# Kernel tuning notes

Measured on AMD Instinct MI355X. Metric: run time of the kernel, lower is better.

Reference implementation:

```python
import jax, jax.numpy as jnp
import numpy as np

N_NODES = 100000
N_EDGES = 1600000
N_FEAT = 128
N_HID = 128


def cheb_conv_k2(x, edge_index, W0, W1, b):
    """PyG ChebConv with K=2, sym norm, lambda_max=2.0.
    Reduces to: out = x @ W0 + (L_hat x) @ W1 + b, where
    L_hat = 2L/lambda_max - I = -D^{-1/2} A D^{-1/2} (diagonal cancels).
    """
    n = x.shape[0]
    row, col = edge_index[0], edge_index[1]
    deg = jax.ops.segment_sum(jnp.ones_like(row, dtype=x.dtype), row, num_segments=n)
    dinv = jnp.where(deg > 0, jax.lax.rsqrt(jnp.maximum(deg, 1.0)), 0.0)
    w = -(dinv[row] * dinv[col])                     # [E] edge weights of L_hat
    tx1 = jax.ops.segment_sum(x[col] * w[:, None], row, num_segments=n)  # [N, F]
    return x @ W0 + tx1 @ W1 + b


def setup_inputs() -> dict:
    key = jax.random.key(0)
    ks = jax.random.split(key, 8)
    glorot = lambda k, fi, fo: jax.random.normal(k, (fi, fo), dtype=jnp.float32) * np.float32(np.sqrt(2.0 / (fi + fo)))
    x = jax.random.normal(ks[0], (N_NODES, N_FEAT), dtype=jnp.float32)
    edge_index = jax.random.randint(ks[1], (2, N_EDGES), 0, N_NODES, dtype=jnp.int64 if jax.config.jax_enable_x64 else jnp.int32)
    return {
        "x": x,
        "edge_index": edge_index,
        "W0_1": glorot(ks[2], N_FEAT, N_HID),
        "W1_1": glorot(ks[3], N_FEAT, N_HID),
        "b1": jnp.zeros((N_HID,), dtype=jnp.float32),
        "W0_2": glorot(ks[4], N_HID, N_HID),
        "W1_2": glorot(ks[5], N_HID, N_HID),
        "b2": jnp.zeros((N_HID,), dtype=jnp.float32),
    }


def reference(x, edge_index, W0_1, W1_1, b1, W0_2, W1_2, b2):
    # eval mode: input Dropout, dropout_adj(p=0.8), and per-layer Dropout are identity
    x1 = jax.nn.relu(cheb_conv_k2(x, edge_index, W0_1, W1_1, b1))
    x2 = jax.nn.relu(cheb_conv_k2(x1, edge_index, W0_2, W1_2, b2))
    # mean of the two layer outputs; outAct is identity
    return (x1 + x2) * 0.5
```

## Files before the change

### kernel.cpp

```cpp
#include <hip/hip_runtime.h>

#define NN 100000
#define NE 1600000
#define NF 128
#define NSTRIP2 (NN / 32)
#define NBUCK ((NN + 127) / 128)
#define CAP 2560
#define CHUNK 8192

typedef __attribute__((ext_vector_type(8))) short short8;
typedef __attribute__((ext_vector_type(4))) float f32x4;

__device__ __forceinline__ unsigned short f2b(float f) {
    union { float f; unsigned int u; } v; v.f = f;
    unsigned int u = v.u;
    unsigned int r = (u + 0x7fffu + ((u >> 16) & 1u)) >> 16;
    return (unsigned short)r;
}
__device__ __forceinline__ unsigned int cvtpk(float lo, float hi) {
    unsigned int r;
    asm("v_cvt_pk_bf16_f32 %0, %1, %2" : "=v"(r) : "v"(lo), "v"(hi));
    return r;
}

__global__ __launch_bounds__(512) void k_bin(const int* __restrict__ row,
                                             const int* __restrict__ col,
                                             int* __restrict__ gcur,
                                             unsigned int* __restrict__ gslab) {
    __shared__ int hist[NBUCK];
    __shared__ int start[NBUCK];
    __shared__ int gbase[NBUCK];
    __shared__ int scanbuf[512];
    __shared__ unsigned int stage[CHUNK];
    __shared__ unsigned short sb[CHUNK];

    const int t = threadIdx.x;
    const int e0 = blockIdx.x * CHUNK;
    const int cnt = min(CHUNK, NE - e0);

    for (int i = t; i < NBUCK; i += 512) hist[i] = 0;
    __syncthreads();
    for (int i = t; i < cnt; i += 512) atomicAdd(&hist[row[e0 + i] >> 7], 1);
    __syncthreads();

    const int b0 = t * 2;
    int s = 0;
#pragma unroll
    for (int k = 0; k < 2; ++k) { int idx = b0 + k; if (idx < NBUCK) s += hist[idx]; }
    scanbuf[t] = s;
    __syncthreads();
    for (int off = 1; off < 512; off <<= 1) {
        int u = t >= off ? scanbuf[t - off] : 0;
        __syncthreads();
        scanbuf[t] += u;
        __syncthreads();
    }
    int run = t > 0 ? scanbuf[t - 1] : 0;
#pragma unroll
    for (int k = 0; k < 2; ++k) {
        int idx = b0 + k;
        if (idx < NBUCK) { start[idx] = run; run += hist[idx]; }
    }
    __syncthreads();

    for (int i = t; i < NBUCK; i += 512) {
        int c = hist[i];
        gbase[i] = c > 0 ? atomicAdd(&gcur[i], c) : 0;
        hist[i] = start[i];
    }
    __syncthreads();

    for (int i = t; i < cnt; i += 512) {
        int r = row[e0 + i];
        int b = r >> 7;
        int p = atomicAdd(&hist[b], 1);
        stage[p] = (unsigned int)col[e0 + i] | ((unsigned int)(r & 127) << 17);
        sb[p] = (unsigned short)b;
    }
    __syncthreads();

    for (int i = t; i < cnt; i += 512) {
        int b = sb[i];
        gslab[gbase[b] + (i - start[b])] = stage[i];
    }
}

__global__ __launch_bounds__(256) void k_csr(const unsigned int* __restrict__ gslab,
                                             const int* __restrict__ gcur,
                                             int* __restrict__ offs,
                                             int* __restrict__ ccol,
                                             float* __restrict__ dinv) {
    __shared__ int rh[128];
    __shared__ int rcur[128];
    __shared__ unsigned int scol[CAP];
    __shared__ int redbuf[256];

    const int b = blockIdx.x;
    const int segbase = b * CAP;
    const int cnt = gcur[b] - segbase;
    const int t = threadIdx.x;

    int partial = 0;
    for (int i = t; i < b; i += 256) partial += gcur[i] - i * CAP;
    redbuf[t] = partial;
    if (t < 128) rh[t] = 0;
    __syncthreads();
    for (int off = 128; off > 0; off >>= 1) {
        if (t < off) redbuf[t] += redbuf[t + off];
        __syncthreads();
    }
    const int csr0 = redbuf[0];

    for (int i = t; i < cnt; i += 256) atomicAdd(&rh[gslab[segbase + i] >> 17], 1);
    __syncthreads();
    if (t == 0) {
        int run = 0;
        for (int r = 0; r < 128; ++r) { rcur[r] = run; run += rh[r]; }
    }
    __syncthreads();

    const int rbase = b * 128;
    if (t < 128 && rbase + t < NN) {
        offs[rbase + t] = csr0 + rcur[t];
        int d = rh[t];
        dinv[rbase + t] = d > 0 ? rsqrtf((float)d) : 0.0f;
    }
    if (b == NBUCK - 1 && t == 0) offs[NN] = NE;
    __syncthreads();

    for (int i = t; i < cnt; i += 256) {
        unsigned int v = gslab[segbase + i];
        int p = atomicAdd(&rcur[v >> 17], 1);
        scol[p] = v & 0x1ffff;
    }
    __syncthreads();
    for (int i = t; i < cnt; i += 256) ccol[csr0 + i] = scol[i];
}

__global__ __launch_bounds__(256) void k_quant(const float* __restrict__ x,
                                               const float* __restrict__ dinv,
                                               unsigned short* __restrict__ xq,
                                               float* __restrict__ dsc,
                                               float* __restrict__ sx) {
    int r = (blockIdx.x * 256 + threadIdx.x) >> 6;
    int lane = threadIdx.x & 63;
    float2 v = ((const float2*)x)[r * 64 + lane];
    float m = fmaxf(fabsf(v.x), fabsf(v.y));
#pragma unroll
    for (int mask = 32; mask; mask >>= 1) m = fmaxf(m, __shfl_xor(m, mask));
    float s = m * (1.0f / 127.0f);
    float inv = m > 0.0f ? 127.0f / m : 0.0f;
    int qx = (int)rintf(v.x * inv) + 128;
    int qy = (int)rintf(v.y * inv) + 128;
    xq[r * 64 + lane] = (unsigned short)(qx | (qy << 8));
    if (lane == 0) { dsc[r] = dinv[r] * s; sx[r] = s; }
}

__global__ __launch_bounds__(256) void k_pack(const float* __restrict__ W01,
                                              const float* __restrict__ W11,
                                              const float* __restrict__ W02,
                                              const float* __restrict__ W12,
                                              unsigned short* __restrict__ WP,
                                              int* __restrict__ gcur) {
    int idx = blockIdx.x * 256 + threadIdx.x;
    if (idx < NBUCK) gcur[idx] = idx * CAP;
    int mi = idx >> 14;
    int e = idx & 16383;
    const float* W = mi == 0 ? W01 : mi == 1 ? W02 : mi == 2 ? W11 : W12;
    int midx = mi == 0 ? 0 : mi == 1 ? 2 : mi == 2 ? 1 : 3;
    int k = e >> 7, n = e & 127;
    int kt = k >> 5, g = (k >> 3) & 3, j = k & 7;
    WP[midx * 16384 + (((kt * 4 + g) * 128 + n) << 3) + j] = f2b(W[e]);
}

__global__ __launch_bounds__(256) void k_gather(const int* __restrict__ offs,
                                                const int* __restrict__ ccol,
                                                const float* __restrict__ dsc,
                                                const float* __restrict__ dinv,
                                                const uint2* __restrict__ xq64,
                                                uint4* __restrict__ txb4,
                                                float qbias) {
    int r = (blockIdx.x * 256 + threadIdx.x) >> 6;
    if (r >= NN) return;
    int lane = threadIdx.x & 63;
    int fl = lane & 15, q = lane >> 4;
    int beg = offs[r], end = offs[r + 1];
    float a0 = 0.f, a1 = 0.f, a2 = 0.f, a3 = 0.f;
    float a4 = 0.f, a5 = 0.f, a6 = 0.f, a7 = 0.f, S = 0.f;
    int j = beg + q;
    for (; j + 12 < end; j += 16) {
        int c0 = ccol[j], c1 = ccol[j + 4], c2 = ccol[j + 8], c3 = ccol[j + 12];
        float w0 = dsc[c0], w1 = dsc[c1], w2 = dsc[c2], w3 = dsc[c3];
        uint2 u0 = xq64[c0 * 16 + fl];
        uint2 u1 = xq64[c1 * 16 + fl];
        uint2 u2 = xq64[c2 * 16 + fl];
        uint2 u3 = xq64[c3 * 16 + fl];
        a0 += w0 * (float)(u0.x & 0xffu)         + w1 * (float)(u1.x & 0xffu)
            + w2 * (float)(u2.x & 0xffu)         + w3 * (float)(u3.x & 0xffu);
        a1 += w0 * (float)((u0.x >> 8) & 0xffu)  + w1 * (float)((u1.x >> 8) & 0xffu)
            + w2 * (float)((u2.x >> 8) & 0xffu)  + w3 * (float)((u3.x >> 8) & 0xffu);
        a2 += w0 * (float)((u0.x >> 16) & 0xffu) + w1 * (float)((u1.x >> 16) & 0xffu)
            + w2 * (float)((u2.x >> 16) & 0xffu) + w3 * (float)((u3.x >> 16) & 0xffu);
        a3 += w0 * (float)(u0.x >> 24)           + w1 * (float)(u1.x >> 24)
            + w2 * (float)(u2.x >> 24)           + w3 * (float)(u3.x >> 24);
        a4 += w0 * (float)(u0.y & 0xffu)         + w1 * (float)(u1.y & 0xffu)
            + w2 * (float)(u2.y & 0xffu)         + w3 * (float)(u3.y & 0xffu);
        a5 += w0 * (float)((u0.y >> 8) & 0xffu)  + w1 * (float)((u1.y >> 8) & 0xffu)
            + w2 * (float)((u2.y >> 8) & 0xffu)  + w3 * (float)((u3.y >> 8) & 0xffu);
        a6 += w0 * (float)((u0.y >> 16) & 0xffu) + w1 * (float)((u1.y >> 16) & 0xffu)
            + w2 * (float)((u2.y >> 16) & 0xffu) + w3 * (float)((u3.y >> 16) & 0xffu);
        a7 += w0 * (float)(u0.y >> 24)           + w1 * (float)(u1.y >> 24)
            + w2 * (float)(u2.y >> 24)           + w3 * (float)(u3.y >> 24);
        S += w0 + w1 + w2 + w3;
    }
    for (; j < end; j += 4) {
        int c = ccol[j];
        float w = dsc[c];
        uint2 u = xq64[c * 16 + fl];
        a0 += w * (float)(u.x & 0xffu);
        a1 += w * (float)((u.x >> 8) & 0xffu);
        a2 += w * (float)((u.x >> 16) & 0xffu);
        a3 += w * (float)(u.x >> 24);
        a4 += w * (float)(u.y & 0xffu);
        a5 += w * (float)((u.y >> 8) & 0xffu);
        a6 += w * (float)((u.y >> 16) & 0xffu);
        a7 += w * (float)(u.y >> 24);
        S += w;
    }
#pragma unroll
    for (int mask = 32; mask >= 16; mask >>= 1) {
        a0 += __shfl_xor(a0, mask); a1 += __shfl_xor(a1, mask);
        a2 += __shfl_xor(a2, mask); a3 += __shfl_xor(a3, mask);
        a4 += __shfl_xor(a4, mask); a5 += __shfl_xor(a5, mask);
        a6 += __shfl_xor(a6, mask); a7 += __shfl_xor(a7, mask);
        S  += __shfl_xor(S, mask);
    }
    if (q == 0) {
        float s = -dinv[r];
        float qb = qbias * S;
        a0 = s * (a0 - qb); a1 = s * (a1 - qb); a2 = s * (a2 - qb); a3 = s * (a3 - qb);
        a4 = s * (a4 - qb); a5 = s * (a5 - qb); a6 = s * (a6 - qb); a7 = s * (a7 - qb);
        uint4 o;
        o.x = cvtpk(a0, a1);
        o.y = cvtpk(a2, a3);
        o.z = cvtpk(a4, a5);
        o.w = cvtpk(a6, a7);
        txb4[r * 16 + fl] = o;
    }
}

__global__ __launch_bounds__(256) void k_mm(const unsigned char* __restrict__ Aq,
                                            const float* __restrict__ s_in,
                                            float qoff,
                                            const unsigned short* __restrict__ Tbf,
                                            const unsigned short* __restrict__ WP0,
                                            const unsigned short* __restrict__ WP1,
                                            const float* __restrict__ bias,
                                            const float* __restrict__ dinv,
                                            float* __restrict__ out,
                                            unsigned char* __restrict__ Qout,
                                            float* __restrict__ dsc_out,
                                            float* __restrict__ s1_out,
                                            int mode) {
    int wid = (blockIdx.x * 256 + threadIdx.x) >> 6;
    if (wid >= NSTRIP2) return;
    int lane = threadIdx.x & 63;
    int g = lane >> 4, m = lane & 15;

    short8 a[2][4], t[2][4];
#pragma unroll
    for (int s = 0; s < 2; ++s) {
        int row = wid * 32 + s * 16 + m;
        float sA = s_in[row];
        float nb = -qoff * sA;
        const unsigned char* Arow = Aq + (size_t)row * NF + g * 8;
        const short8* Tfr = (const short8*)(Tbf + (size_t)row * NF + g * 8);
#pragma unroll
        for (int kt = 0; kt < 4; ++kt) {
            uint2 u = *(const uint2*)(Arow + kt * 32);
            float f0 = fmaf((float)(u.x & 0xffu), sA, nb);
            float f1 = fmaf((float)((u.x >> 8) & 0xffu), sA, nb);
            float f2 = fmaf((float)((u.x >> 16) & 0xffu), sA, nb);
            float f3 = fmaf((float)(u.x >> 24), sA, nb);
            float f4 = fmaf((float)(u.y & 0xffu), sA, nb);
            float f5 = fmaf((float)((u.y >> 8) & 0xffu), sA, nb);
            float f6 = fmaf((float)((u.y >> 16) & 0xffu), sA, nb);
            float f7 = fmaf((float)(u.y >> 24), sA, nb);
            union { uint4 q; short8 v; } cc;
            cc.q.x = cvtpk(f0, f1);
            cc.q.y = cvtpk(f2, f3);
            cc.q.z = cvtpk(f4, f5);
            cc.q.w = cvtpk(f6, f7);
            a[s][kt] = cc.v;
            t[s][kt] = Tfr[kt * 4];
        }
    }

    const short8* B0 = (const short8*)WP0 + g * 128 + m;
    const short8* B1 = (const short8*)WP1 + g * 128 + m;

    f32x4 acc[2][8];
#pragma unroll
    for (int nt = 0; nt < 8; ++nt) {
        float b = bias[nt * 16 + m];
#pragma unroll
        for (int s = 0; s < 2; ++s) {
            acc[s][nt][0] = b; acc[s][nt][1] = b; acc[s][nt][2] = b; acc[s][nt][3] = b;
        }
    }

#pragma unroll
    for (int nt = 0; nt < 8; ++nt) {
#pragma unroll
        for (int kt = 0; kt < 4; ++kt) {
            short8 b0 = B0[kt * 512 + nt * 16];
            short8 b1 = B1[kt * 512 + nt * 16];
#pragma unroll
            for (int s = 0; s < 2; ++s) {
                acc[s][nt] = __builtin_amdgcn_mfma_f32_16x16x32_bf16(a[s][kt], b0, acc[s][nt], 0, 0, 0);
                acc[s][nt] = __builtin_amdgcn_mfma_f32_16x16x32_bf16(t[s][kt], b1, acc[s][nt], 0, 0, 0);
            }
        }
    }

#pragma unroll
    for (int s = 0; s < 2; ++s)
#pragma unroll
        for (int nt = 0; nt < 8; ++nt)
#pragma unroll
            for (int r = 0; r < 4; ++r) acc[s][nt][r] = fmaxf(acc[s][nt][r], 0.0f);

    if (mode == 0) {
#pragma unroll
        for (int s = 0; s < 2; ++s) {
            int rbase = wid * 32 + s * 16 + g * 4;
            float mr[4] = {0.0f, 0.0f, 0.0f, 0.0f};
#pragma unroll
            for (int nt = 0; nt < 8; ++nt)
#pragma unroll
                for (int r = 0; r < 4; ++r) mr[r] = fmaxf(mr[r], acc[s][nt][r]);
#pragma unroll
            for (int mask = 1; mask < 16; mask <<= 1)
#pragma unroll
                for (int r = 0; r < 4; ++r) mr[r] = fmaxf(mr[r], __shfl_xor(mr[r], mask));

            float inv[4], s1v[4];
#pragma unroll
            for (int r = 0; r < 4; ++r) {
                s1v[r] = mr[r] * (1.0f / 255.0f);
                inv[r] = mr[r] > 0.0f ? 255.0f / mr[r] : 0.0f;
            }
#pragma unroll
            for (int nt = 0; nt < 8; ++nt) {
                int c = nt * 16 + m;
#pragma unroll
                for (int r = 0; r < 4; ++r) {
                    int qv = (int)rintf(acc[s][nt][r] * inv[r]);
                    qv = qv > 255 ? 255 : qv;
                    Qout[(size_t)(rbase + r) * NF + c] = (unsigned char)qv;
                }
            }
            if (m == 0) {
#pragma unroll
                for (int r = 0; r < 4; ++r) {
                    s1_out[rbase + r] = s1v[r];
                    dsc_out[rbase + r] = dinv[rbase + r] * s1v[r];
                }
            }
        }
    } else {
#pragma unroll
        for (int s = 0; s < 2; ++s) {
            int rbase = wid * 32 + s * 16 + g * 4;
            float sR[4];
#pragma unroll
            for (int r = 0; r < 4; ++r) sR[r] = s_in[rbase + r];
#pragma unroll
            for (int nt = 0; nt < 8; ++nt) {
                int c = nt * 16 + m;
#pragma unroll
                for (int r = 0; r < 4; ++r) {
                    size_t o = (size_t)(rbase + r) * NF + c;
                    float x1v = sR[r] * (float)Aq[o];
                    out[o] = 0.5f * (x1v + acc[s][nt][r]);
                }
            }
        }
    }
}

extern "C" void kernel_launch(void* const* d_in, const int* in_sizes, int n_in,
                              void* d_out, int out_size, void* d_ws, size_t ws_size,
                              hipStream_t stream) {
    const float* x   = (const float*)d_in[0];
    const int*   ei  = (const int*)d_in[1];
    const float* W01 = (const float*)d_in[2];
    const float* W11 = (const float*)d_in[3];
    const float* b1  = (const float*)d_in[4];
    const float* W02 = (const float*)d_in[5];
    const float* W12 = (const float*)d_in[6];
    const float* b2  = (const float*)d_in[7];
    float* out = (float*)d_out;

    const int* row = ei;
    const int* col = ei + NE;

    char* ws = (char*)d_ws;
    int*            gcur  = (int*)(ws);
    float*          dinv  = (float*)(ws + 6400);
    int*            offs  = (int*)(ws + 406400);
    int*            ccol  = (int*)(ws + 806416);
    unsigned short* WP    = (unsigned short*)(ws + 7206416);
    float*          dsc   = (float*)(ws + 7337488);
    float*          s1a   = (float*)(ws + 7737488);
    float*          sx    = (float*)(ws + 8137488);
    unsigned short* xq    = (unsigned short*)(ws + 8537488);
    unsigned int*   txb   = (unsigned int*)(ws + 21337488);
    unsigned int*   gslab = (unsigned int*)(ws + 21337488);

    unsigned char*  xq8 = (unsigned char*)xq;
    unsigned short* WP01 = WP;
    unsigned short* WP11 = WP + 16384;
    unsigned short* WP02 = WP + 32768;
    unsigned short* WP12 = WP + 49152;

    k_pack <<<(4 * 16384) / 256, 256, 0, stream>>>(W01, W11, W02, W12, WP, gcur);
    k_bin  <<<(NE + CHUNK - 1) / CHUNK, 512, 0, stream>>>(row, col, gcur, gslab);
    k_csr  <<<NBUCK, 256, 0, stream>>>(gslab, gcur, offs, ccol, dinv);

    k_quant<<<(NN * 64) / 256, 256, 0, stream>>>(x, dinv, xq, dsc, sx);

    const int gatherBlocks = (NN * 64) / 256;
    const int mmBlocks = (NSTRIP2 * 64 + 255) / 256;

    k_gather<<<gatherBlocks, 256, 0, stream>>>(offs, ccol, dsc, dinv,
                                               (const uint2*)xq, (uint4*)txb, 128.0f);
    k_mm    <<<mmBlocks, 256, 0, stream>>>(xq8, sx, 128.0f, (const unsigned short*)txb,
                                           WP01, WP11, b1, dinv, out, xq8, dsc, s1a, 0);

    k_gather<<<gatherBlocks, 256, 0, stream>>>(offs, ccol, dsc, dinv,
                                               (const uint2*)xq, (uint4*)txb, 0.0f);
    k_mm    <<<mmBlocks, 256, 0, stream>>>(xq8, s1a, 0.0f, (const unsigned short*)txb,
                                           WP02, WP12, b2, dinv, out, xq8, dsc, s1a, 1);
}
```

Baseline: 226.9 us.

## Stage packed weights in LDS for matmul and batch gather tail loads

The matmul kernel now copies both packed bf16 weight matrices (64 KB) into shared memory once per block and reads MFMA B fragments from LDS instead of global memory. The gather kernel's scalar remainder loop is replaced by one unrolled step that issues up to three independent neighbour loads together. Out-of-range slots point at a sentinel row NN whose dsc entry is set to zero, so workspace offsets shift to make room for it. The LDS staging adds a per-block copy and a large shared allocation that can reduce occupancy. The tail rewrite assumes at most three leftover edges per lane.

Result: faster. 207.2 us (-8.7%).

```diff
diff --git a/kernel.cpp b/kernel.cpp
--- a/kernel.cpp
+++ b/kernel.cpp
@@ -153,7 +153,9 @@
     int qx = (int)rintf(v.x * inv) + 128;
     int qy = (int)rintf(v.y * inv) + 128;
     xq[r * 64 + lane] = (unsigned short)(qx | (qy << 8));
-    if (lane == 0) { dsc[r] = dinv[r] * s; sx[r] = s; }
+    if (lane == 0) dsc[r] = dinv[r] * s;
+    if (lane == 1) sx[r] = dinv[r] != 0.0f || true ? s : s;
+    if (r == 0 && lane == 2) dsc[NN] = 0.0f;
 }
 
 __global__ __launch_bounds__(256) void k_pack(const float* __restrict__ W01,
@@ -213,19 +215,31 @@
             + w2 * (float)(u2.y >> 24)           + w3 * (float)(u3.y >> 24);
         S += w0 + w1 + w2 + w3;
     }
-    for (; j < end; j += 4) {
-        int c = ccol[j];
-        float w = dsc[c];
-        uint2 u = xq64[c * 16 + fl];
-        a0 += w * (float)(u.x & 0xffu);
-        a1 += w * (float)((u.x >> 8) & 0xffu);
-        a2 += w * (float)((u.x >> 16) & 0xffu);
-        a3 += w * (float)(u.x >> 24);
-        a4 += w * (float)(u.y & 0xffu);
-        a5 += w * (float)((u.y >> 8) & 0xffu);
-        a6 += w * (float)((u.y >> 16) & 0xffu);
-        a7 += w * (float)(u.y >> 24);
-        S += w;
+    if (j < end) {
+        int c0 = ccol[j];
+        int c1 = j + 4 < end ? ccol[j + 4] : NN;
+        int c2 = j + 8 < end ? ccol[j + 8] : NN;
+        float w0 = dsc[c0], w1 = dsc[c1], w2 = dsc[c2];
+        uint2 u0 = xq64[c0 * 16 + fl];
+        uint2 u1 = xq64[c1 * 16 + fl];
+        uint2 u2 = xq64[c2 * 16 + fl];
+        a0 += w0 * (float)(u0.x & 0xffu)         + w1 * (float)(u1.x & 0xffu)
+            + w2 * (float)(u2.x & 0xffu);
+        a1 += w0 * (float)((u0.x >> 8) & 0xffu)  + w1 * (float)((u1.x >> 8) & 0xffu)
+            + w2 * (float)((u2.x >> 8) & 0xffu);
+        a2 += w0 * (float)((u0.x >> 16) & 0xffu) + w1 * (float)((u1.x >> 16) & 0xffu)
+            + w2 * (float)((u2.x >> 16) & 0xffu);
+        a3 += w0 * (float)(u0.x >> 24)           + w1 * (float)(u1.x >> 24)
+            + w2 * (float)(u2.x >> 24);
+        a4 += w0 * (float)(u0.y & 0xffu)         + w1 * (float)(u1.y & 0xffu)
+            + w2 * (float)(u2.y & 0xffu);
+        a5 += w0 * (float)((u0.y >> 8) & 0xffu)  + w1 * (float)((u1.y >> 8) & 0xffu)
+            + w2 * (float)((u2.y >> 8) & 0xffu);
+        a6 += w0 * (float)((u0.y >> 16) & 0xffu) + w1 * (float)((u1.y >> 16) & 0xffu)
+            + w2 * (float)((u2.y >> 16) & 0xffu);
+        a7 += w0 * (float)(u0.y >> 24)           + w1 * (float)(u1.y >> 24)
+            + w2 * (float)(u2.y >> 24);
+        S += w0 + w1 + w2;
     }
 #pragma unroll
     for (int mask = 32; mask >= 16; mask >>= 1) {
@@ -262,6 +276,18 @@
                                             float* __restrict__ dsc_out,
                                             float* __restrict__ s1_out,
                                             int mode) {
+    __shared__ short8 Bs0[2048];
+    __shared__ short8 Bs1[2048];
+    {
+        const short8* W0f = (const short8*)WP0;
+        const short8* W1f = (const short8*)WP1;
+        for (int i = threadIdx.x; i < 2048; i += 256) {
+            Bs0[i] = W0f[i];
+            Bs1[i] = W1f[i];
+        }
+    }
+    __syncthreads();
+
     int wid = (blockIdx.x * 256 + threadIdx.x) >> 6;
     if (wid >= NSTRIP2) return;
     int lane = threadIdx.x & 63;
@@ -296,8 +322,7 @@
         }
     }
 
-    const short8* B0 = (const short8*)WP0 + g * 128 + m;
-    const short8* B1 = (const short8*)WP1 + g * 128 + m;
+    const int bbase = g * 128 + m;
 
     f32x4 acc[2][8];
 #pragma unroll
@@ -313,8 +338,8 @@
     for (int nt = 0; nt < 8; ++nt) {
 #pragma unroll
         for (int kt = 0; kt < 4; ++kt) {
-            short8 b0 = B0[kt * 512 + nt * 16];
-            short8 b1 = B1[kt * 512 + nt * 16];
+            short8 b0 = Bs0[bbase + kt * 512 + nt * 16];
+            short8 b1 = Bs1[bbase + kt * 512 + nt * 16];
 #pragma unroll
             for (int s = 0; s < 2; ++s) {
                 acc[s][nt] = __builtin_amdgcn_mfma_f32_16x16x32_bf16(a[s][kt], b0, acc[s][nt], 0, 0, 0);
@@ -412,11 +437,11 @@
     int*            ccol  = (int*)(ws + 806416);
     unsigned short* WP    = (unsigned short*)(ws + 7206416);
     float*          dsc   = (float*)(ws + 7337488);
-    float*          s1a   = (float*)(ws + 7737488);
-    float*          sx    = (float*)(ws + 8137488);
-    unsigned short* xq    = (unsigned short*)(ws + 8537488);
-    unsigned int*   txb   = (unsigned int*)(ws + 21337488);
-    unsigned int*   gslab = (unsigned int*)(ws + 21337488);
+    float*          s1a   = (float*)(ws + 7737504);
+    float*          sx    = (float*)(ws + 8137504);
+    unsigned short* xq    = (unsigned short*)(ws + 8537504);
+    unsigned int*   txb   = (unsigned int*)(ws + 21337632);
+    unsigned int*   gslab = (unsigned int*)(ws + 21337632);
 
     unsigned char*  xq8 = (unsigned char*)xq;
     unsigned short* WP01 = WP;
```
